# Kernel tuning notes

Hardware: AMD Instinct MI355X
Metric: run time of the kernel (lower is better)

Reference implementation:

```python
import jax, jax.numpy as jnp
import numpy as np

ENC, DEC, B, S = 1024, 1024, 32, 2048


def setup_inputs() -> dict:
    key = jax.random.key(0)
    k1, k2, k3, k4, k5, k6 = jax.random.split(key, 6)
    scale_attn = 1.0 / np.sqrt(ENC + DEC)
    return {
        "decoder_hidden": jax.random.normal(k1, (B, DEC), dtype=jnp.float32),
        "encoder_outputs": jax.random.normal(k2, (B, S, ENC), dtype=jnp.float32),
        "mask": jax.random.randint(k3, (B, S), 0, 2, dtype=jnp.int32),
        "W_attn": jax.random.normal(k4, (ENC + DEC, DEC), dtype=jnp.float32) * scale_attn,
        "b_attn": jax.random.normal(k5, (DEC,), dtype=jnp.float32) * 0.02,
        "v_w": jax.random.normal(k6, (DEC,), dtype=jnp.float32) * (1.0 / np.sqrt(DEC)),
    }


def reference(decoder_hidden, encoder_outputs, mask, W_attn, b_attn, v_w):
    # Split cat((dec_exp, enc)) @ W into two GEMMs (same math, no repeat/concat).
    dec_dim = decoder_hidden.shape[-1]
    W_dec = W_attn[:dec_dim]      # [DEC, DEC]
    W_enc = W_attn[dec_dim:]      # [ENC, DEC]
    dec_proj = decoder_hidden @ W_dec                      # [B, DEC]
    enc_proj = jnp.einsum("bse,ed->bsd", encoder_outputs, W_enc)  # [B, S, DEC]
    energy = jnp.tanh(dec_proj[:, None, :] + enc_proj + b_attn)   # [B, S, DEC]
    scores = jnp.einsum("bsd,d->bs", energy, v_w)                 # [B, S]
    scores = jnp.where(mask == 0, -1e9, scores)
    attn_weights = jax.nn.softmax(scores, axis=1)                 # [B, S]
    context = jnp.einsum("bs,bse->be", attn_weights, encoder_outputs)  # [B, ENC]
    return (context, attn_weights)
```

## Files before the change

kernel.cpp:

```cpp
#include <hip/hip_runtime.h>
#include <hip/hip_bf16.h>
#include <cstdint>


#define ENCD 1024
#define DECD 1024
#define BATCH 32
#define SEQ 2048
#define MTOT (BATCH * SEQ)
#define KDIM 1024
#define NDIM 1024

typedef __attribute__((ext_vector_type(4))) float f32x4;
typedef __attribute__((ext_vector_type(8))) __bf16 bf16x8;
typedef __attribute__((ext_vector_type(8))) unsigned short u16x8;

__device__ __forceinline__ unsigned short f2bf(float f) {
  unsigned int u = __builtin_bit_cast(unsigned int, f);
  u += 0x7fffu + ((u >> 16) & 1u);
  return (unsigned short)(u >> 16);
}

__device__ __forceinline__ float bf2f(unsigned short h) {
  return __builtin_bit_cast(float, (unsigned int)h << 16);
}

__device__ __forceinline__ void async_lds16(const unsigned short* g, unsigned short* l) {
  __builtin_amdgcn_global_load_lds(
      (const __attribute__((address_space(1))) unsigned int*)g,
      (__attribute__((address_space(3))) unsigned int*)l, 16, 0, 0);
}

__device__ __forceinline__ void barx() {
  __builtin_amdgcn_s_barrier();
  asm volatile("" ::: "memory");
}

template <int N>
__device__ __forceinline__ void waitv() {
  if constexpr (N == 0) {
    asm volatile("s_waitcnt vmcnt(0)" ::: "memory");
  } else if constexpr (N == 2) {
    asm volatile("s_waitcnt vmcnt(2)" ::: "memory");
  } else {
    asm volatile("s_waitcnt vmcnt(4)" ::: "memory");
  }
}

__global__ void conv_bf16_k(const float* __restrict__ src, unsigned short* __restrict__ dst) {
  const long i = ((long)blockIdx.x * 256 + threadIdx.x) * 8;
  const f32x4 f0 = *(const f32x4*)(src + i);
  const f32x4 f1 = *(const f32x4*)(src + i + 4);
  u16x8 v;
  v[0] = f2bf(f0[0]); v[1] = f2bf(f0[1]); v[2] = f2bf(f0[2]); v[3] = f2bf(f0[3]);
  v[4] = f2bf(f1[0]); v[5] = f2bf(f1[1]); v[6] = f2bf(f1[2]); v[7] = f2bf(f1[3]);
  *(u16x8*)(dst + i) = v;
}

__global__ void wt_k(const float* __restrict__ W, unsigned short* __restrict__ Wt) {
  __shared__ unsigned short t[64][65];
  const int k0 = blockIdx.x * 64, n0 = blockIdx.y * 64;
  const int tx = threadIdx.x & 63, ty = threadIdx.x >> 6;
#pragma unroll
  for (int i = 0; i < 16; ++i) {
    const int k = ty + i * 4;
    t[k][tx] = f2bf(W[(long)(DECD + k0 + k) * NDIM + n0 + tx]);
  }
  __syncthreads();
#pragma unroll
  for (int i = 0; i < 16; ++i) {
    const int n = ty + i * 4;
    Wt[(long)(n0 + n) * KDIM + k0 + tx] = t[tx][n];
  }
}

__global__ void dec1_k(const float* __restrict__ dec, const float* __restrict__ W,
                       float* __restrict__ part) {
  const int idx = blockIdx.x * 256 + threadIdx.x;
  const int kc = blockIdx.y;
  const int b = idx >> 10;
  const int n = idx & 1023;
  const float* d = dec + b * DECD + kc * 128;
  const float* w = W + (long)(kc * 128) * NDIM + n;
  float acc = 0.f;
#pragma unroll 8
  for (int k = 0; k < 128; ++k) acc = fmaf(d[k], w[(long)k * NDIM], acc);
  part[kc * 32768 + idx] = acc;
}

__global__ void dec2_k(const float* __restrict__ part, const float* __restrict__ bias,
                       float* __restrict__ dp) {
  const int idx = blockIdx.x * 256 + threadIdx.x;
  float s = bias[idx & 1023];
#pragma unroll
  for (int kc = 0; kc < 8; ++kc) s += part[kc * 32768 + idx];
  dp[idx] = s;
}

template <bool STG, int W1, int W2>
__device__ __forceinline__ void gtile(
    const unsigned short* Acur, const unsigned short* Bcur,
    unsigned short* Anxt, unsigned short* Bnxt,
    const unsigned short* Ab, const unsigned short* Bb, int k0n,
    int wm, int wn, int wv, int quad, int l15, int srow, int schunk,
    f32x4 (&acc)[8][4], bf16x8 (&aF)[4][2], bf16x8 (&bF)[4][2]) {
  const int sw = l15 & 7;
#define RDF(buf, row, h) \
  __builtin_bit_cast(bf16x8, *(const u16x8*)&(buf)[(row) * 64 + ((((h) * 4 + quad) ^ sw) * 8)])
#pragma unroll
  for (int mt = 0; mt < 4; ++mt) {
    const int row = wm * 128 + mt * 16 + l15;
    aF[mt][0] = RDF(Acur, row, 0);
    aF[mt][1] = RDF(Acur, row, 1);
  }
#pragma unroll
  for (int nt = 0; nt < 2; ++nt) {
    const int row = wn * 64 + nt * 16 + l15;
    bF[nt][0] = RDF(Bcur, row, 0);
    bF[nt][1] = RDF(Bcur, row, 1);
  }
  if (STG) {
    async_lds16(Bb + (size_t)(wv * 16 + srow) * KDIM + k0n + schunk * 8, Bnxt + (wv * 16) * 64);
    async_lds16(Bb + (size_t)(wv * 16 + 8 + srow) * KDIM + k0n + schunk * 8, Bnxt + (wv * 16 + 8) * 64);
  }
  barx();
  __builtin_amdgcn_s_setprio(1);
#pragma unroll
  for (int h = 0; h < 2; ++h)
#pragma unroll
    for (int mt = 0; mt < 4; ++mt)
#pragma unroll
      for (int nt = 0; nt < 2; ++nt)
        acc[mt][nt] = __builtin_amdgcn_mfma_f32_16x16x32_bf16(aF[mt][h], bF[nt][h], acc[mt][nt], 0, 0, 0);
  __builtin_amdgcn_s_setprio(0);
  barx();
#pragma unroll
  for (int nt = 2; nt < 4; ++nt) {
    const int row = wn * 64 + nt * 16 + l15;
    bF[nt][0] = RDF(Bcur, row, 0);
    bF[nt][1] = RDF(Bcur, row, 1);
  }
  if (STG) {
    async_lds16(Bb + (size_t)(128 + wv * 16 + srow) * KDIM + k0n + schunk * 8, Bnxt + (128 + wv * 16) * 64);
    async_lds16(Bb + (size_t)(128 + wv * 16 + 8 + srow) * KDIM + k0n + schunk * 8, Bnxt + (128 + wv * 16 + 8) * 64);
  }
  waitv<W1>();
  barx();
  __builtin_amdgcn_s_setprio(1);
#pragma unroll
  for (int h = 0; h < 2; ++h)
#pragma unroll
    for (int mt = 0; mt < 4; ++mt)
#pragma unroll
      for (int nt = 0; nt < 2; ++nt)
        acc[mt][2 + nt] = __builtin_amdgcn_mfma_f32_16x16x32_bf16(aF[mt][h], bF[2 + nt][h], acc[mt][2 + nt], 0, 0, 0);
  __builtin_amdgcn_s_setprio(0);
  barx();
#pragma unroll
  for (int mt = 0; mt < 4; ++mt) {
    const int row = wm * 128 + (4 + mt) * 16 + l15;
    aF[mt][0] = RDF(Acur, row, 0);
    aF[mt][1] = RDF(Acur, row, 1);
  }
  if (STG) {
    async_lds16(Ab + (size_t)(wv * 8 + srow) * KDIM + k0n + schunk * 8, Anxt + (wv * 8) * 64);
    async_lds16(Ab + (size_t)(128 + wv * 8 + srow) * KDIM + k0n + schunk * 8, Anxt + (128 + wv * 8) * 64);
  }
  barx();
  __builtin_amdgcn_s_setprio(1);
#pragma unroll
  for (int h = 0; h < 2; ++h)
#pragma unroll
    for (int mt = 0; mt < 4; ++mt)
#pragma unroll
      for (int nt = 0; nt < 2; ++nt)
        acc[4 + mt][nt] = __builtin_amdgcn_mfma_f32_16x16x32_bf16(aF[mt][h], bF[nt][h], acc[4 + mt][nt], 0, 0, 0);
  __builtin_amdgcn_s_setprio(0);
  barx();
  if (STG) {
    async_lds16(Ab + (size_t)(64 + wv * 8 + srow) * KDIM + k0n + schunk * 8, Anxt + (64 + wv * 8) * 64);
    async_lds16(Ab + (size_t)(192 + wv * 8 + srow) * KDIM + k0n + schunk * 8, Anxt + (192 + wv * 8) * 64);
  }
  waitv<W2>();
  barx();
  __builtin_amdgcn_s_setprio(1);
#pragma unroll
  for (int h = 0; h < 2; ++h)
#pragma unroll
    for (int mt = 0; mt < 4; ++mt)
#pragma unroll
      for (int nt = 0; nt < 2; ++nt)
        acc[4 + mt][2 + nt] = __builtin_amdgcn_mfma_f32_16x16x32_bf16(aF[mt][h], bF[2 + nt][h], acc[4 + mt][2 + nt], 0, 0, 0);
  __builtin_amdgcn_s_setprio(0);
  barx();
#undef RDF
}

__global__ __launch_bounds__(512, 2) void gemm8_k(
    const unsigned short* __restrict__ Abf, const unsigned short* __restrict__ Wt,
    const float* __restrict__ dp, const float* __restrict__ vw,
    float* __restrict__ sp) {
  __shared__ unsigned short sA[2][256 * 64];
  __shared__ unsigned short sB[2][256 * 64];
  const int tid = threadIdx.x;
  const int lane = tid & 63;
  const int wv = tid >> 6;
  const int wm = wv >> 2, wn = wv & 3;
  const int quad = lane >> 4;
  const int l15 = lane & 15;
  const int srow = lane >> 3;
  const int schunk = (lane & 7) ^ srow;

  const int bn = blockIdx.x;
  const int bm = blockIdx.y;
  const int n0 = bn * 256;
  const int row0 = bm * 256;
  const int bidx = bm >> 3;

  const unsigned short* Ab = Abf + (size_t)row0 * KDIM;
  const unsigned short* Bb = Wt + (size_t)n0 * KDIM;

  const f32x4 zz = {0.f, 0.f, 0.f, 0.f};
  f32x4 acc[8][4];
#pragma unroll
  for (int i = 0; i < 8; ++i)
#pragma unroll
    for (int j = 0; j < 4; ++j) acc[i][j] = zz;
  bf16x8 aF[4][2], bF[4][2];

  async_lds16(Bb + (size_t)(wv * 16 + srow) * KDIM + schunk * 8, &sB[0][(wv * 16) * 64]);
  async_lds16(Bb + (size_t)(wv * 16 + 8 + srow) * KDIM + schunk * 8, &sB[0][(wv * 16 + 8) * 64]);
  async_lds16(Bb + (size_t)(128 + wv * 16 + srow) * KDIM + schunk * 8, &sB[0][(128 + wv * 16) * 64]);
  async_lds16(Bb + (size_t)(128 + wv * 16 + 8 + srow) * KDIM + schunk * 8, &sB[0][(128 + wv * 16 + 8) * 64]);
  async_lds16(Ab + (size_t)(wv * 8 + srow) * KDIM + schunk * 8, &sA[0][(wv * 8) * 64]);
  async_lds16(Ab + (size_t)(128 + wv * 8 + srow) * KDIM + schunk * 8, &sA[0][(128 + wv * 8) * 64]);
  async_lds16(Ab + (size_t)(64 + wv * 8 + srow) * KDIM + schunk * 8, &sA[0][(64 + wv * 8) * 64]);
  async_lds16(Ab + (size_t)(192 + wv * 8 + srow) * KDIM + schunk * 8, &sA[0][(192 + wv * 8) * 64]);
  waitv<2>();
  barx();

  for (int it = 0; it < 7; ++it) {
    const int kb = it * 2;
    gtile<true, 4, 2>(sA[0], sB[0], sA[1], sB[1], Ab, Bb, (kb + 1) * 64,
                      wm, wn, wv, quad, l15, srow, schunk, acc, aF, bF);
    gtile<true, 4, 2>(sA[1], sB[1], sA[0], sB[0], Ab, Bb, (kb + 2) * 64,
                      wm, wn, wv, quad, l15, srow, schunk, acc, aF, bF);
  }
  gtile<true, 4, 2>(sA[0], sB[0], sA[1], sB[1], Ab, Bb, 15 * 64,
                    wm, wn, wv, quad, l15, srow, schunk, acc, aF, bF);
  gtile<false, 0, 0>(sA[1], sB[1], sA[0], sB[0], Ab, Bb, 0,
                     wm, wn, wv, quad, l15, srow, schunk, acc, aF, bF);

  float vv[4], dv[4];
#pragma unroll
  for (int nt = 0; nt < 4; ++nt) {
    const int n = n0 + wn * 64 + nt * 16 + l15;
    vv[nt] = vw[n];
    dv[nt] = dp[bidx * NDIM + n];
  }
  float* sRed = (float*)sA;
#pragma unroll
  for (int mt = 0; mt < 8; ++mt) {
#pragma unroll
    for (int r = 0; r < 4; ++r) {
      float s = 0.f;
#pragma unroll
      for (int nt = 0; nt < 4; ++nt) {
        float x = acc[mt][nt][r] + dv[nt];
        x = fminf(fmaxf(x, -10.f), 10.f);
        const float e = __expf(2.f * x);
        s += (e - 1.f) * __builtin_amdgcn_rcpf(e + 1.f) * vv[nt];
      }
      s += __shfl_xor(s, 1);
      s += __shfl_xor(s, 2);
      s += __shfl_xor(s, 4);
      s += __shfl_xor(s, 8);
      if (l15 == 0) sRed[wn * 256 + wm * 128 + mt * 16 + quad * 4 + r] = s;
    }
  }
  __syncthreads();
  if (tid < 256) {
    const float s4 = sRed[tid] + sRed[256 + tid] + sRed[512 + tid] + sRed[768 + tid];
    sp[(size_t)bn * MTOT + row0 + tid] = s4;
  }
}

__global__ void softmax_part_k(const float* __restrict__ sp, const int* __restrict__ mask,
                               float* __restrict__ attn) {
  const int b = blockIdx.x;
  const int tid = threadIdx.x;
  const int w = tid >> 6;
  __shared__ float redm[4], reds[4];
  const int* mrow = mask + b * SEQ;
  float vals[8];
  float mx = -3.0e38f;
#pragma unroll
  for (int i = 0; i < 8; ++i) {
    const int s = tid + i * 256;
    float v = 0.f;
#pragma unroll
    for (int bn = 0; bn < 4; ++bn) v += sp[(size_t)bn * MTOT + b * SEQ + s];
    if (mrow[s] == 0) v = -1.0e9f;
    vals[i] = v;
    mx = fmaxf(mx, v);
  }
#pragma unroll
  for (int off = 1; off < 64; off <<= 1) mx = fmaxf(mx, __shfl_xor(mx, off));
  if ((tid & 63) == 0) redm[w] = mx;
  __syncthreads();
  mx = fmaxf(fmaxf(redm[0], redm[1]), fmaxf(redm[2], redm[3]));
  float sum = 0.f;
#pragma unroll
  for (int i = 0; i < 8; ++i) {
    vals[i] = __expf(vals[i] - mx);
    sum += vals[i];
  }
#pragma unroll
  for (int off = 1; off < 64; off <<= 1) sum += __shfl_xor(sum, off);
  if ((tid & 63) == 0) reds[w] = sum;
  __syncthreads();
  sum = reds[0] + reds[1] + reds[2] + reds[3];
  const float inv = 1.0f / sum;
#pragma unroll
  for (int i = 0; i < 8; ++i) attn[b * SEQ + tid + i * 256] = vals[i] * inv;
}

__global__ void ctx1_k(const float* __restrict__ attn, const unsigned short* __restrict__ Abf,
                       float* __restrict__ part) {
  __shared__ float red[128 * 8];
  const int sc = blockIdx.x;
  const int b = blockIdx.y;
  const int half = threadIdx.x >> 7;
  const int te = threadIdx.x & 127;
  const int e0 = te * 8;
  const int sbase = sc * 128 + half * 64;
  const float* arow = attn + b * SEQ + sbase;
  const unsigned short* base = Abf + (size_t)(b * SEQ + sbase) * ENCD + e0;
  float acc[8] = {0.f, 0.f, 0.f, 0.f, 0.f, 0.f, 0.f, 0.f};
#pragma unroll 8
  for (int s = 0; s < 64; ++s) {
    const float w = arow[s];
    const u16x8 v = *(const u16x8*)(base + (size_t)s * ENCD);
#pragma unroll
    for (int j = 0; j < 8; ++j) acc[j] = fmaf(w, bf2f(v[j]), acc[j]);
  }
  if (half == 1) {
#pragma unroll
    for (int j = 0; j < 8; ++j) red[te * 8 + j] = acc[j];
  }
  __syncthreads();
  if (half == 0) {
#pragma unroll
    for (int j = 0; j < 8; ++j) acc[j] += red[te * 8 + j];
    float* dst = part + (size_t)sc * (BATCH * ENCD) + b * ENCD + e0;
    *(f32x4*)dst = *(f32x4*)&acc[0];
    *(f32x4*)(dst + 4) = *(f32x4*)&acc[4];
  }
}

__global__ void ctx2_k(const float* __restrict__ part, float* __restrict__ ctx) {
  const int i = blockIdx.x * 256 + threadIdx.x;
  float s = 0.f;
#pragma unroll
  for (int c = 0; c < 16; ++c) s += part[(size_t)c * (BATCH * ENCD) + i];
  ctx[i] = s;
}

__global__ void dec_proj_k2(const float* __restrict__ dec, const float* __restrict__ W,
                            float* __restrict__ dp) {
  const int idx = blockIdx.x * 256 + threadIdx.x;
  const int kc = blockIdx.y;
  const int b = idx >> 10;
  const int n = idx & 1023;
  const float* d = dec + b * DECD + kc * 128;
  const float* w = W + (long)(kc * 128) * NDIM + n;
  float acc = 0.f;
#pragma unroll 8
  for (int k = 0; k < 128; ++k) acc = fmaf(d[k], w[(long)k * NDIM], acc);
  atomicAdd(&dp[idx], acc);
}

__global__ __launch_bounds__(256, 3) void gemm_scores_bf16(
    const unsigned short* __restrict__ Abf, const unsigned short* __restrict__ Wt,
    const float* __restrict__ dp, const float* __restrict__ bias,
    const float* __restrict__ vw, float* __restrict__ scores) {
  __shared__ unsigned short sA[128 * 64];
  __shared__ unsigned short sB[128 * 64];
  const int tid = threadIdx.x;
  const int lane = tid & 63;
  const int wave = tid >> 6;
  const int wm = wave >> 1, wn = wave & 1;
  const int quad = lane >> 4;
  const int l15 = lane & 15;
  const int bn = blockIdx.x, bm = blockIdx.y;
  const int n0 = bn * 128, row0 = bm * 128, bidx = bm >> 4;
  const int srow = lane >> 3;
  const int schunk = (lane & 7) ^ srow;
  const f32x4 zz = {0.f, 0.f, 0.f, 0.f};
  f32x4 acc[4][4];
#pragma unroll
  for (int i = 0; i < 4; ++i)
#pragma unroll
    for (int j = 0; j < 4; ++j) acc[i][j] = zz;
  for (int kt = 0; kt < 16; ++kt) {
    const int k0 = kt * 64;
    __syncthreads();
#pragma unroll
    for (int i = 0; i < 4; ++i) {
      const int r = wave * 32 + i * 8 + srow;
      async_lds16(Abf + (size_t)(row0 + r) * KDIM + k0 + schunk * 8,
                  &sA[(wave * 32 + i * 8) * 64]);
      async_lds16(Wt + (size_t)(n0 + r) * KDIM + k0 + schunk * 8,
                  &sB[(wave * 32 + i * 8) * 64]);
    }
    __syncthreads();
#pragma unroll
    for (int h = 0; h < 2; ++h) {
      bf16x8 af[4], bf[4];
      const int slot = ((h * 4 + quad) ^ (l15 & 7)) * 8;
#pragma unroll
      for (int t = 0; t < 4; ++t) {
        af[t] = __builtin_bit_cast(bf16x8, *(const u16x8*)&sA[(wm * 64 + t * 16 + l15) * 64 + slot]);
        bf[t] = __builtin_bit_cast(bf16x8, *(const u16x8*)&sB[(wn * 64 + t * 16 + l15) * 64 + slot]);
      }
#pragma unroll
      for (int mt = 0; mt < 4; ++mt)
#pragma unroll
        for (int nt = 0; nt < 4; ++nt)
          acc[mt][nt] = __builtin_amdgcn_mfma_f32_16x16x32_bf16(
              af[mt], bf[nt], acc[mt][nt], 0, 0, 0);
    }
  }
  float vv[4], dv[4];
#pragma unroll
  for (int nt = 0; nt < 4; ++nt) {
    const int n = n0 + wn * 64 + nt * 16 + l15;
    vv[nt] = vw[n];
    dv[nt] = dp[bidx * NDIM + n] + bias[n];
  }
#pragma unroll
  for (int mt = 0; mt < 4; ++mt) {
#pragma unroll
    for (int r = 0; r < 4; ++r) {
      float s = 0.f;
#pragma unroll
      for (int nt = 0; nt < 4; ++nt) {
        float x = acc[mt][nt][r] + dv[nt];
        x = fminf(fmaxf(x, -10.f), 10.f);
        const float e = __expf(2.f * x);
        s += (e - 1.f) * __builtin_amdgcn_rcpf(e + 1.f) * vv[nt];
      }
      s += __shfl_xor(s, 1);
      s += __shfl_xor(s, 2);
      s += __shfl_xor(s, 4);
      s += __shfl_xor(s, 8);
      if (l15 == 0) atomicAdd(&scores[row0 + wm * 64 + mt * 16 + quad * 4 + r], s);
    }
  }
}

__global__ __launch_bounds__(256, 2) void gemm_scores_f32(
    const float* __restrict__ Ag, const unsigned short* __restrict__ Wt,
    const float* __restrict__ dp, const float* __restrict__ bias,
    const float* __restrict__ vw, float* __restrict__ scores) {
  __shared__ unsigned short sA[128 * 64];
  __shared__ unsigned short sB[128 * 64];
  const int tid = threadIdx.x;
  const int lane = tid & 63;
  const int wave = tid >> 6;
  const int wm = wave >> 1, wn = wave & 1;
  const int quad = lane >> 4;
  const int l15 = lane & 15;
  const int bn = blockIdx.x, bm = blockIdx.y;
  const int n0 = bn * 128, row0 = bm * 128, bidx = bm >> 4;
  const int sr = tid >> 3, sc = tid & 7;
  const f32x4 zz = {0.f, 0.f, 0.f, 0.f};
  f32x4 acc[4][4];
#pragma unroll
  for (int i = 0; i < 4; ++i)
#pragma unroll
    for (int j = 0; j < 4; ++j) acc[i][j] = zz;
  for (int kt = 0; kt < 16; ++kt) {
    const int k0 = kt * 64;
    __syncthreads();
#pragma unroll
    for (int j = 0; j < 4; ++j) {
      const int r = sr + 32 * j;
      const int c = sc ^ (r & 7);
      const float* src = Ag + (long)(row0 + r) * KDIM + (k0 + c * 8);
      f32x4 f0 = *(const f32x4*)src;
      f32x4 f1 = *(const f32x4*)(src + 4);
      u16x8 v;
      v[0] = f2bf(f0[0]); v[1] = f2bf(f0[1]); v[2] = f2bf(f0[2]); v[3] = f2bf(f0[3]);
      v[4] = f2bf(f1[0]); v[5] = f2bf(f1[1]); v[6] = f2bf(f1[2]); v[7] = f2bf(f1[3]);
      *(u16x8*)&sA[r * 64 + sc * 8] = v;
      *(u16x8*)&sB[r * 64 + sc * 8] = *(const u16x8*)(Wt + (long)(n0 + r) * KDIM + (k0 + c * 8));
    }
    __syncthreads();
#pragma unroll
    for (int h = 0; h < 2; ++h) {
      const int cs = ((h * 4 + quad) ^ (lane & 7)) * 8;
      bf16x8 af[4], bf[4];
#pragma unroll
      for (int t = 0; t < 4; ++t) {
        af[t] = __builtin_bit_cast(bf16x8, *(const u16x8*)&sA[(wm * 64 + t * 16 + l15) * 64 + cs]);
        bf[t] = __builtin_bit_cast(bf16x8, *(const u16x8*)&sB[(wn * 64 + t * 16 + l15) * 64 + cs]);
      }
#pragma unroll
      for (int mt = 0; mt < 4; ++mt)
#pragma unroll
        for (int nt = 0; nt < 4; ++nt)
          acc[mt][nt] = __builtin_amdgcn_mfma_f32_16x16x32_bf16(
              af[mt], bf[nt], acc[mt][nt], 0, 0, 0);
    }
  }
  float vv[4], dv[4];
#pragma unroll
  for (int nt = 0; nt < 4; ++nt) {
    const int n = n0 + wn * 64 + nt * 16 + l15;
    vv[nt] = vw[n];
    dv[nt] = dp[bidx * NDIM + n] + bias[n];
  }
#pragma unroll
  for (int mt = 0; mt < 4; ++mt) {
#pragma unroll
    for (int r = 0; r < 4; ++r) {
      float s = 0.f;
#pragma unroll
      for (int nt = 0; nt < 4; ++nt) {
        float x = acc[mt][nt][r] + dv[nt];
        x = fminf(fmaxf(x, -10.f), 10.f);
        const float e = __expf(2.f * x);
        s += (e - 1.f) * __builtin_amdgcn_rcpf(e + 1.f) * vv[nt];
      }
      s += __shfl_xor(s, 1);
      s += __shfl_xor(s, 2);
      s += __shfl_xor(s, 4);
      s += __shfl_xor(s, 8);
      if (l15 == 0) atomicAdd(&scores[row0 + wm * 64 + mt * 16 + quad * 4 + r], s);
    }
  }
}

__global__ void softmax_k(float* __restrict__ sc, const int* __restrict__ mask) {
  const int b = blockIdx.x;
  const int tid = threadIdx.x;
  const int w = tid >> 6;
  __shared__ float redm[4], reds[4];
  float* row = sc + b * SEQ;
  const int* mrow = mask + b * SEQ;
  float vals[8];
  float mx = -3.0e38f;
#pragma unroll
  for (int i = 0; i < 8; ++i) {
    const int s = tid + i * 256;
    float v = row[s];
    if (mrow[s] == 0) v = -1.0e9f;
    vals[i] = v;
    mx = fmaxf(mx, v);
  }
#pragma unroll
  for (int off = 1; off < 64; off <<= 1) mx = fmaxf(mx, __shfl_xor(mx, off));
  if ((tid & 63) == 0) redm[w] = mx;
  __syncthreads();
  mx = fmaxf(fmaxf(redm[0], redm[1]), fmaxf(redm[2], redm[3]));
  float sum = 0.f;
#pragma unroll
  for (int i = 0; i < 8; ++i) {
    vals[i] = __expf(vals[i] - mx);
    sum += vals[i];
  }
#pragma unroll
  for (int off = 1; off < 64; off <<= 1) sum += __shfl_xor(sum, off);
  if ((tid & 63) == 0) reds[w] = sum;
  __syncthreads();
  sum = reds[0] + reds[1] + reds[2] + reds[3];
  const float inv = 1.0f / sum;
#pragma unroll
  for (int i = 0; i < 8; ++i) row[tid + i * 256] = vals[i] * inv;
}

__global__ void context_k(const float* __restrict__ attn, const float* __restrict__ enc,
                          float* __restrict__ ctx) {
  const int b = blockIdx.y;
  const int s0 = blockIdx.x * 32;
  const int e = threadIdx.x * 4;
  const float* arow = attn + b * SEQ + s0;
  const float* ebase = enc + (long)(b * SEQ + s0) * ENCD + e;
  f32x4 acc = {0.f, 0.f, 0.f, 0.f};
#pragma unroll 8
  for (int s = 0; s < 32; ++s) {
    const float w = arow[s];
    const f32x4 v = *(const f32x4*)(ebase + (long)s * ENCD);
    acc += w * v;
  }
  float* dst = ctx + b * ENCD + e;
  atomicAdd(dst + 0, acc[0]);
  atomicAdd(dst + 1, acc[1]);
  atomicAdd(dst + 2, acc[2]);
  atomicAdd(dst + 3, acc[3]);
}

extern "C" void kernel_launch(void* const* d_in, const int* in_sizes, int n_in,
                              void* d_out, int out_size, void* d_ws, size_t ws_size,
                              hipStream_t stream) {
  (void)in_sizes; (void)n_in; (void)out_size;
  const float* dec  = (const float*)d_in[0];
  const float* enc  = (const float*)d_in[1];
  const int*   mask = (const int*)d_in[2];
  const float* W    = (const float*)d_in[3];
  const float* bias = (const float*)d_in[4];
  const float* vw   = (const float*)d_in[5];

  float* ctx  = (float*)d_out;
  float* attn = (float*)d_out + BATCH * ENCD;
  unsigned short* Wt  = (unsigned short*)d_ws;
  unsigned short* Abf = (unsigned short*)((char*)d_ws + (2ull << 20));
  float* shared = (float*)((char*)d_ws + (130ull << 20));

  const size_t needA = (132ull << 20);
  const size_t needB = (2ull << 20) + ((size_t)MTOT * KDIM * 2);

  wt_k<<<dim3(16, 16), 256, 0, stream>>>(W, Wt);
  if (ws_size >= needA) {
    dec1_k<<<dim3(128, 8), 256, 0, stream>>>(dec, W, shared);
    dec2_k<<<128, 256, 0, stream>>>(shared, bias, ctx);
    conv_bf16_k<<<32768, 256, 0, stream>>>(enc, Abf);
    gemm8_k<<<dim3(4, 256), 512, 0, stream>>>(Abf, Wt, ctx, vw, shared);
    softmax_part_k<<<32, 256, 0, stream>>>(shared, mask, attn);
    ctx1_k<<<dim3(16, 32), 256, 0, stream>>>(attn, Abf, shared);
    ctx2_k<<<128, 256, 0, stream>>>(shared, ctx);
  } else if (ws_size >= needB) {
    hipMemsetAsync(attn, 0, (size_t)MTOT * sizeof(float), stream);
    hipMemsetAsync(ctx, 0, (size_t)(BATCH * NDIM) * sizeof(float), stream);
    dec_proj_k2<<<dim3(128, 8), 256, 0, stream>>>(dec, W, ctx);
    conv_bf16_k<<<32768, 256, 0, stream>>>(enc, Abf);
    gemm_scores_bf16<<<dim3(8, 512), 256, 0, stream>>>(Abf, Wt, ctx, bias, vw, attn);
    softmax_k<<<32, 256, 0, stream>>>(attn, mask);
    hipMemsetAsync(ctx, 0, (size_t)(BATCH * ENCD) * sizeof(float), stream);
    context_k<<<dim3(64, 32), 256, 0, stream>>>(attn, enc, ctx);
  } else {
    hipMemsetAsync(attn, 0, (size_t)MTOT * sizeof(float), stream);
    hipMemsetAsync(ctx, 0, (size_t)(BATCH * NDIM) * sizeof(float), stream);
    dec_proj_k2<<<dim3(128, 8), 256, 0, stream>>>(dec, W, ctx);
    gemm_scores_f32<<<dim3(8, 512), 256, 0, stream>>>(enc, Wt, ctx, bias, vw, attn);
    softmax_k<<<32, 256, 0, stream>>>(attn, mask);
    hipMemsetAsync(ctx, 0, (size_t)(BATCH * ENCD) * sizeof(float), stream);
    context_k<<<dim3(64, 32), 256, 0, stream>>>(attn, enc, ctx);
  }
}
```

Baseline: 595.8 us.

## Fuse prep kernels, restage GEMM pipeline, remap blocks by XCD, fuse softmax+context

Merges the weight transpose, decoder projection (now a single full-K pass with bias) and bf16 conversion into one launch. Restructures the GEMM so each buffer is refilled in place with a tile two k-steps ahead and waits at vmcnt(8). It also remaps block indices so that blocks sharing an XCD work on related rows. Softmax and the context reduction are fused into one kernel where each block recomputes the softmax for its batch row. These changes cut launch count and partial-sum round trips, at the cost of redundant softmax work, a serial 1024-long decoder dot product, and a more delicate LDS reuse scheme.

```diff
diff --git a/kernel.cpp b/kernel.cpp
--- a/kernel.cpp
+++ b/kernel.cpp
@@ -40,10 +40,8 @@
 __device__ __forceinline__ void waitv() {
   if constexpr (N == 0) {
     asm volatile("s_waitcnt vmcnt(0)" ::: "memory");
-  } else if constexpr (N == 2) {
-    asm volatile("s_waitcnt vmcnt(2)" ::: "memory");
   } else {
-    asm volatile("s_waitcnt vmcnt(4)" ::: "memory");
+    asm volatile("s_waitcnt vmcnt(8)" ::: "memory");
   }
 }
 
@@ -74,34 +72,63 @@
   }
 }
 
-__global__ void dec1_k(const float* __restrict__ dec, const float* __restrict__ W,
-                       float* __restrict__ part) {
-  const int idx = blockIdx.x * 256 + threadIdx.x;
-  const int kc = blockIdx.y;
-  const int b = idx >> 10;
-  const int n = idx & 1023;
-  const float* d = dec + b * DECD + kc * 128;
-  const float* w = W + (long)(kc * 128) * NDIM + n;
-  float acc = 0.f;
+__global__ __launch_bounds__(256) void prep_k(
+    const float* __restrict__ dec, const float* __restrict__ enc,
+    const float* __restrict__ W, const float* __restrict__ bias,
+    float* __restrict__ dp, unsigned short* __restrict__ Wt,
+    unsigned short* __restrict__ Abf) {
+  const int gb = blockIdx.x;
+  const int tid = threadIdx.x;
+  if (gb < 128) {
+    const int b = gb >> 2;
+    const int n = (gb & 3) * 256 + tid;
+    const float* d = dec + b * DECD;
+    const float* w = W + n;
+    float acc = bias[n];
 #pragma unroll 8
-  for (int k = 0; k < 128; ++k) acc = fmaf(d[k], w[(long)k * NDIM], acc);
-  part[kc * 32768 + idx] = acc;
-}
-
-__global__ void dec2_k(const float* __restrict__ part, const float* __restrict__ bias,
-                       float* __restrict__ dp) {
-  const int idx = blockIdx.x * 256 + threadIdx.x;
-  float s = bias[idx & 1023];
-#pragma unroll
-  for (int kc = 0; kc < 8; ++kc) s += part[kc * 32768 + idx];
-  dp[idx] = s;
-}
-
-template <bool STG, int W1, int W2>
-__device__ __forceinline__ void gtile(
-    const unsigned short* Acur, const unsigned short* Bcur,
-    unsigned short* Anxt, unsigned short* Bnxt,
-    const unsigned short* Ab, const unsigned short* Bb, int k0n,
+    for (int k = 0; k < 1024; ++k) acc = fmaf(d[k], w[(size_t)k * NDIM], acc);
+    dp[b * NDIM + n] = acc;
+  } else if (gb < 384) {
+    __shared__ unsigned short t[64][65];
+    const int g2 = gb - 128;
+    const int k0 = (g2 & 15) * 64, n0 = (g2 >> 4) * 64;
+    const int tx = tid & 63, ty = tid >> 6;
+#pragma unroll
+    for (int i = 0; i < 16; ++i) {
+      const int k = ty + i * 4;
+      t[k][tx] = f2bf(W[(size_t)(DECD + k0 + k) * NDIM + n0 + tx]);
+    }
+    __syncthreads();
+#pragma unroll
+    for (int i = 0; i < 16; ++i) {
+      const int n = ty + i * 4;
+      Wt[(size_t)(n0 + n) * KDIM + k0 + tx] = t[tx][n];
+    }
+  } else {
+    const long i = ((long)(gb - 384) * 256 + tid) * 8;
+    const f32x4 f0 = *(const f32x4*)(enc + i);
+    const f32x4 f1 = *(const f32x4*)(enc + i + 4);
+    u16x8 v;
+    v[0] = f2bf(f0[0]); v[1] = f2bf(f0[1]); v[2] = f2bf(f0[2]); v[3] = f2bf(f0[3]);
+    v[4] = f2bf(f1[0]); v[5] = f2bf(f1[1]); v[6] = f2bf(f1[2]); v[7] = f2bf(f1[3]);
+    *(u16x8*)(Abf + i) = v;
+  }
+}
+
+
+__device__ __forceinline__ void stage4(const unsigned short* gbase, unsigned short* lbase,
+                                       int wv, int srow, int schunk, int k0) {
+#pragma unroll
+  for (int j = 0; j < 4; ++j) {
+    async_lds16(gbase + (size_t)(j * 64 + wv * 8 + srow) * KDIM + k0 + schunk * 8,
+                lbase + (j * 64 + wv * 8) * 64);
+  }
+}
+
+template <bool STG, int BW>
+__device__ __forceinline__ void gtile2(
+    unsigned short* sAc, unsigned short* sBc,
+    const unsigned short* Ab, const unsigned short* Bb, int k2,
     int wm, int wn, int wv, int quad, int l15, int srow, int schunk,
     f32x4 (&acc)[8][4], bf16x8 (&aF)[4][2], bf16x8 (&bF)[4][2]) {
   const int sw = l15 & 7;
@@ -110,18 +137,14 @@
 #pragma unroll
   for (int mt = 0; mt < 4; ++mt) {
     const int row = wm * 128 + mt * 16 + l15;
-    aF[mt][0] = RDF(Acur, row, 0);
-    aF[mt][1] = RDF(Acur, row, 1);
+    aF[mt][0] = RDF(sAc, row, 0);
+    aF[mt][1] = RDF(sAc, row, 1);
   }
 #pragma unroll
   for (int nt = 0; nt < 2; ++nt) {
     const int row = wn * 64 + nt * 16 + l15;
-    bF[nt][0] = RDF(Bcur, row, 0);
-    bF[nt][1] = RDF(Bcur, row, 1);
-  }
-  if (STG) {
-    async_lds16(Bb + (size_t)(wv * 16 + srow) * KDIM + k0n + schunk * 8, Bnxt + (wv * 16) * 64);
-    async_lds16(Bb + (size_t)(wv * 16 + 8 + srow) * KDIM + k0n + schunk * 8, Bnxt + (wv * 16 + 8) * 64);
+    bF[nt][0] = RDF(sBc, row, 0);
+    bF[nt][1] = RDF(sBc, row, 1);
   }
   barx();
   __builtin_amdgcn_s_setprio(1);
@@ -137,14 +160,9 @@
 #pragma unroll
   for (int nt = 2; nt < 4; ++nt) {
     const int row = wn * 64 + nt * 16 + l15;
-    bF[nt][0] = RDF(Bcur, row, 0);
-    bF[nt][1] = RDF(Bcur, row, 1);
-  }
-  if (STG) {
-    async_lds16(Bb + (size_t)(128 + wv * 16 + srow) * KDIM + k0n + schunk * 8, Bnxt + (128 + wv * 16) * 64);
-    async_lds16(Bb + (size_t)(128 + wv * 16 + 8 + srow) * KDIM + k0n + schunk * 8, Bnxt + (128 + wv * 16 + 8) * 64);
-  }
-  waitv<W1>();
+    bF[nt][0] = RDF(sBc, row, 0);
+    bF[nt][1] = RDF(sBc, row, 1);
+  }
   barx();
   __builtin_amdgcn_s_setprio(1);
 #pragma unroll
@@ -159,13 +177,10 @@
 #pragma unroll
   for (int mt = 0; mt < 4; ++mt) {
     const int row = wm * 128 + (4 + mt) * 16 + l15;
-    aF[mt][0] = RDF(Acur, row, 0);
-    aF[mt][1] = RDF(Acur, row, 1);
-  }
-  if (STG) {
-    async_lds16(Ab + (size_t)(wv * 8 + srow) * KDIM + k0n + schunk * 8, Anxt + (wv * 8) * 64);
-    async_lds16(Ab + (size_t)(128 + wv * 8 + srow) * KDIM + k0n + schunk * 8, Anxt + (128 + wv * 8) * 64);
-  }
+    aF[mt][0] = RDF(sAc, row, 0);
+    aF[mt][1] = RDF(sAc, row, 1);
+  }
+  if (STG) stage4(Bb, sBc, wv, srow, schunk, k2);
   barx();
   __builtin_amdgcn_s_setprio(1);
 #pragma unroll
@@ -177,11 +192,8 @@
         acc[4 + mt][nt] = __builtin_amdgcn_mfma_f32_16x16x32_bf16(aF[mt][h], bF[nt][h], acc[4 + mt][nt], 0, 0, 0);
   __builtin_amdgcn_s_setprio(0);
   barx();
-  if (STG) {
-    async_lds16(Ab + (size_t)(64 + wv * 8 + srow) * KDIM + k0n + schunk * 8, Anxt + (64 + wv * 8) * 64);
-    async_lds16(Ab + (size_t)(192 + wv * 8 + srow) * KDIM + k0n + schunk * 8, Anxt + (192 + wv * 8) * 64);
-  }
-  waitv<W2>();
+  if (STG) stage4(Ab, sAc, wv, srow, schunk, k2);
+  waitv<BW>();
   barx();
   __builtin_amdgcn_s_setprio(1);
 #pragma unroll
@@ -211,8 +223,11 @@
   const int srow = lane >> 3;
   const int schunk = (lane & 7) ^ srow;
 
-  const int bn = blockIdx.x;
-  const int bm = blockIdx.y;
+  const int f = blockIdx.x + (blockIdx.y << 2);
+  const int xcd = f & 7;
+  const int c = f >> 3;
+  const int bn = c & 3;
+  const int bm = xcd + ((c >> 2) << 3);
   const int n0 = bn * 256;
   const int row0 = bm * 256;
   const int bidx = bm >> 3;
@@ -228,28 +243,23 @@
     for (int j = 0; j < 4; ++j) acc[i][j] = zz;
   bf16x8 aF[4][2], bF[4][2];
 
-  async_lds16(Bb + (size_t)(wv * 16 + srow) * KDIM + schunk * 8, &sB[0][(wv * 16) * 64]);
-  async_lds16(Bb + (size_t)(wv * 16 + 8 + srow) * KDIM + schunk * 8, &sB[0][(wv * 16 + 8) * 64]);
-  async_lds16(Bb + (size_t)(128 + wv * 16 + srow) * KDIM + schunk * 8, &sB[0][(128 + wv * 16) * 64]);
-  async_lds16(Bb + (size_t)(128 + wv * 16 + 8 + srow) * KDIM + schunk * 8, &sB[0][(128 + wv * 16 + 8) * 64]);
-  async_lds16(Ab + (size_t)(wv * 8 + srow) * KDIM + schunk * 8, &sA[0][(wv * 8) * 64]);
-  async_lds16(Ab + (size_t)(128 + wv * 8 + srow) * KDIM + schunk * 8, &sA[0][(128 + wv * 8) * 64]);
-  async_lds16(Ab + (size_t)(64 + wv * 8 + srow) * KDIM + schunk * 8, &sA[0][(64 + wv * 8) * 64]);
-  async_lds16(Ab + (size_t)(192 + wv * 8 + srow) * KDIM + schunk * 8, &sA[0][(192 + wv * 8) * 64]);
-  waitv<2>();
-  barx();
-
-  for (int it = 0; it < 7; ++it) {
-    const int kb = it * 2;
-    gtile<true, 4, 2>(sA[0], sB[0], sA[1], sB[1], Ab, Bb, (kb + 1) * 64,
-                      wm, wn, wv, quad, l15, srow, schunk, acc, aF, bF);
-    gtile<true, 4, 2>(sA[1], sB[1], sA[0], sB[0], Ab, Bb, (kb + 2) * 64,
-                      wm, wn, wv, quad, l15, srow, schunk, acc, aF, bF);
-  }
-  gtile<true, 4, 2>(sA[0], sB[0], sA[1], sB[1], Ab, Bb, 15 * 64,
+  stage4(Bb, sB[0], wv, srow, schunk, 0);
+  stage4(Ab, sA[0], wv, srow, schunk, 0);
+  stage4(Bb, sB[1], wv, srow, schunk, 64);
+  stage4(Ab, sA[1], wv, srow, schunk, 64);
+  waitv<8>();
+  barx();
+
+  for (int t = 0; t < 14; t += 2) {
+    gtile2<true, 8>(sA[0], sB[0], Ab, Bb, (t + 2) * 64,
                     wm, wn, wv, quad, l15, srow, schunk, acc, aF, bF);
-  gtile<false, 0, 0>(sA[1], sB[1], sA[0], sB[0], Ab, Bb, 0,
-                     wm, wn, wv, quad, l15, srow, schunk, acc, aF, bF);
+    gtile2<true, 8>(sA[1], sB[1], Ab, Bb, (t + 3) * 64,
+                    wm, wn, wv, quad, l15, srow, schunk, acc, aF, bF);
+  }
+  gtile2<false, 0>(sA[0], sB[0], Ab, Bb, 0,
+                   wm, wn, wv, quad, l15, srow, schunk, acc, aF, bF);
+  gtile2<false, 0>(sA[1], sB[1], Ab, Bb, 0,
+                   wm, wn, wv, quad, l15, srow, schunk, acc, aF, bF);
 
   float vv[4], dv[4];
 #pragma unroll
@@ -285,12 +295,17 @@
   }
 }
 
-__global__ void softmax_part_k(const float* __restrict__ sp, const int* __restrict__ mask,
-                               float* __restrict__ attn) {
-  const int b = blockIdx.x;
+__global__ __launch_bounds__(256) void sm_ctx_k(
+    const float* __restrict__ sp, const int* __restrict__ mask,
+    const unsigned short* __restrict__ Abf,
+    float* __restrict__ attn, float* __restrict__ ctx) {
+  __shared__ float a_s[SEQ];
+  __shared__ float red[16][16][8];
+  __shared__ float redm[4], reds[4];
+  const int ec = blockIdx.x;
+  const int b = blockIdx.y;
   const int tid = threadIdx.x;
   const int w = tid >> 6;
-  __shared__ float redm[4], reds[4];
   const int* mrow = mask + b * SEQ;
   float vals[8];
   float mx = -3.0e38f;
@@ -299,7 +314,7 @@
     const int s = tid + i * 256;
     float v = 0.f;
 #pragma unroll
-    for (int bn = 0; bn < 4; ++bn) v += sp[(size_t)bn * MTOT + b * SEQ + s];
+    for (int p = 0; p < 4; ++p) v += sp[(size_t)p * MTOT + b * SEQ + s];
     if (mrow[s] == 0) v = -1.0e9f;
     vals[i] = v;
     mx = fmaxf(mx, v);
@@ -322,48 +337,34 @@
   sum = reds[0] + reds[1] + reds[2] + reds[3];
   const float inv = 1.0f / sum;
 #pragma unroll
-  for (int i = 0; i < 8; ++i) attn[b * SEQ + tid + i * 256] = vals[i] * inv;
-}
-
-__global__ void ctx1_k(const float* __restrict__ attn, const unsigned short* __restrict__ Abf,
-                       float* __restrict__ part) {
-  __shared__ float red[128 * 8];
-  const int sc = blockIdx.x;
-  const int b = blockIdx.y;
-  const int half = threadIdx.x >> 7;
-  const int te = threadIdx.x & 127;
-  const int e0 = te * 8;
-  const int sbase = sc * 128 + half * 64;
-  const float* arow = attn + b * SEQ + sbase;
-  const unsigned short* base = Abf + (size_t)(b * SEQ + sbase) * ENCD + e0;
+  for (int i = 0; i < 8; ++i) {
+    const float av = vals[i] * inv;
+    a_s[tid + i * 256] = av;
+    if (ec == 0) attn[b * SEQ + tid + i * 256] = av;
+  }
+  __syncthreads();
+  const int sg = tid >> 4, es = tid & 15;
+  const int e0 = ec * 128 + es * 8;
+  const unsigned short* base = Abf + (size_t)(b * SEQ) * ENCD + e0;
   float acc[8] = {0.f, 0.f, 0.f, 0.f, 0.f, 0.f, 0.f, 0.f};
-#pragma unroll 8
-  for (int s = 0; s < 64; ++s) {
-    const float w = arow[s];
+#pragma unroll 4
+  for (int k = 0; k < 128; ++k) {
+    const int s = sg + k * 16;
+    const float wgt = a_s[s];
     const u16x8 v = *(const u16x8*)(base + (size_t)s * ENCD);
 #pragma unroll
-    for (int j = 0; j < 8; ++j) acc[j] = fmaf(w, bf2f(v[j]), acc[j]);
-  }
-  if (half == 1) {
-#pragma unroll
-    for (int j = 0; j < 8; ++j) red[te * 8 + j] = acc[j];
-  }
-  __syncthreads();
-  if (half == 0) {
-#pragma unroll
-    for (int j = 0; j < 8; ++j) acc[j] += red[te * 8 + j];
-    float* dst = part + (size_t)sc * (BATCH * ENCD) + b * ENCD + e0;
-    *(f32x4*)dst = *(f32x4*)&acc[0];
-    *(f32x4*)(dst + 4) = *(f32x4*)&acc[4];
-  }
-}
-
-__global__ void ctx2_k(const float* __restrict__ part, float* __restrict__ ctx) {
-  const int i = blockIdx.x * 256 + threadIdx.x;
-  float s = 0.f;
-#pragma unroll
-  for (int c = 0; c < 16; ++c) s += part[(size_t)c * (BATCH * ENCD) + i];
-  ctx[i] = s;
+    for (int j = 0; j < 8; ++j) acc[j] = fmaf(wgt, bf2f(v[j]), acc[j]);
+  }
+#pragma unroll
+  for (int j = 0; j < 8; ++j) red[sg][es][j] = acc[j];
+  __syncthreads();
+  if (tid < 128) {
+    const int es2 = tid >> 3, j = tid & 7;
+    float ssum = 0.f;
+#pragma unroll
+    for (int g = 0; g < 16; ++g) ssum += red[g][es2][j];
+    ctx[b * ENCD + ec * 128 + es2 * 8 + j] = ssum;
+  }
 }
 
 __global__ void dec_proj_k2(const float* __restrict__ dec, const float* __restrict__ W,
@@ -621,16 +622,12 @@
   const size_t needA = (132ull << 20);
   const size_t needB = (2ull << 20) + ((size_t)MTOT * KDIM * 2);
 
-  wt_k<<<dim3(16, 16), 256, 0, stream>>>(W, Wt);
   if (ws_size >= needA) {
-    dec1_k<<<dim3(128, 8), 256, 0, stream>>>(dec, W, shared);
-    dec2_k<<<128, 256, 0, stream>>>(shared, bias, ctx);
-    conv_bf16_k<<<32768, 256, 0, stream>>>(enc, Abf);
+    prep_k<<<384 + 32768, 256, 0, stream>>>(dec, enc, W, bias, ctx, Wt, Abf);
     gemm8_k<<<dim3(4, 256), 512, 0, stream>>>(Abf, Wt, ctx, vw, shared);
-    softmax_part_k<<<32, 256, 0, stream>>>(shared, mask, attn);
-    ctx1_k<<<dim3(16, 32), 256, 0, stream>>>(attn, Abf, shared);
-    ctx2_k<<<128, 256, 0, stream>>>(shared, ctx);
+    sm_ctx_k<<<dim3(8, 32), 256, 0, stream>>>(shared, mask, Abf, attn, ctx);
   } else if (ws_size >= needB) {
+    wt_k<<<dim3(16, 16), 256, 0, stream>>>(W, Wt);
     hipMemsetAsync(attn, 0, (size_t)MTOT * sizeof(float), stream);
     hipMemsetAsync(ctx, 0, (size_t)(BATCH * NDIM) * sizeof(float), stream);
     dec_proj_k2<<<dim3(128, 8), 256, 0, stream>>>(dec, W, ctx);
@@ -640,6 +637,7 @@
     hipMemsetAsync(ctx, 0, (size_t)(BATCH * ENCD) * sizeof(float), stream);
     context_k<<<dim3(64, 32), 256, 0, stream>>>(attn, enc, ctx);
   } else {
+    wt_k<<<dim3(16, 16), 256, 0, stream>>>(W, Wt);
     hipMemsetAsync(attn, 0, (size_t)MTOT * sizeof(float), stream);
     hipMemsetAsync(ctx, 0, (size_t)(BATCH * NDIM) * sizeof(float), stream);
     dec_proj_k2<<<dim3(128, 8), 256, 0, stream>>>(dec, W, ctx);
```

New measurement: 584.5 us. About the same (-1.9%).
